# Performance work log

Hardware: AMD Instinct MI355X
Metric: run time of the kernel (lower is better)

The kernel has to match this reference:

```python
import jax, jax.numpy as jnp
import numpy as np

EPS = 1e-8

def _masked_mean_summary(h, m):
    # h: [B,D,Nx,T], m: [B,1,Nx,T] -> s: [B,Nx,D]
    msum = jnp.clip(jnp.sum(m, axis=-1), 1.0, None)          # [B,1,Nx]
    s = jnp.sum(h * m, axis=-1) / msum                       # [B,D,Nx]
    return jnp.transpose(s, (0, 2, 1))                       # [B,Nx,D]

def _cosine_alpha(s, prototypes):
    # s: [B,Nx,D], prototypes: [K,D] -> softmax cosine sims [B,Nx,K]
    s_n = s / jnp.clip(jnp.linalg.norm(s, axis=-1, keepdims=True), 1e-12, None)
    p_n = prototypes / jnp.clip(jnp.linalg.norm(prototypes, axis=-1, keepdims=True), 1e-12, None)
    sim = jnp.einsum('bnd,kd->bnk', s_n, p_n)
    return jax.nn.softmax(sim, axis=-1)

def setup_inputs() -> dict:
    key = jax.random.key(0)
    k1, k2, k3 = jax.random.split(key, 3)
    B, D, N, T = 4, 64, 2048, 64
    N_obs, K = 1024, 32
    h_time = jax.random.normal(k1, (B, D, N, T), dtype=jnp.float32)
    mask = jax.random.uniform(k2, (B, 1, N, T), dtype=jnp.float32)
    idx_obs = jnp.arange(N_obs, dtype=jnp.int64)
    prototypes = jax.random.normal(k3, (K, D), dtype=jnp.float32)
    return {"h_time": h_time, "mask": mask, "idx_obs": idx_obs, "prototypes": prototypes}

def reference(h_time, mask, idx_obs, prototypes):
    B, D, N, T = h_time.shape
    # --- observed-node routing ---
    h_obs = h_time[:, :, idx_obs, :]                          # [B,D,No,T]
    mask_obs = mask[:, :, idx_obs, :]                         # [B,1,No,T]
    s_obs = _masked_mean_summary(h_obs, mask_obs)             # [B,No,D]
    alpha_obs = _cosine_alpha(s_obs, prototypes)              # [B,No,K]
    # --- prototype timeseries aggregation (fused broadcast-reduce) ---
    # torch materializes [B,K,D,No,T]; equivalent contraction over No:
    H_num = jnp.einsum('bnk,bdnt->bkdt', alpha_obs, h_obs)    # [B,K,D,T]
    # weights_sum over No is sum_n alpha (independent of t), clamp 1e-8
    denom = jnp.clip(jnp.sum(alpha_obs, axis=1), EPS, None)   # [B,K]
    H_prototypes = H_num / denom[:, :, None, None]            # [B,K,D,T]
    # --- impute unobserved nodes ---
    # compute summaries/routing for ALL nodes, then select unobserved slots
    s_all = _masked_mean_summary(h_time, mask)                # [B,N,D]
    alpha_all = _cosine_alpha(s_all, prototypes)              # [B,N,K]
    imputed = jnp.einsum('bnk,bkdt->bdnt', alpha_all, H_prototypes)  # [B,D,N,T]
    obs_node = jnp.zeros((N,), dtype=bool).at[idx_obs].set(True)
    h_spatial = jnp.where(obs_node[None, None, :, None], h_time, imputed)
    return h_spatial
```

## Files before the change

kernel.cpp:

```cpp
#include <hip/hip_runtime.h>

#define BB   4
#define DD   64
#define NN   2048
#define TT   64
#define NOBS 1024
#define KK   32
#define EPSF 1e-8f

#define S_OFF     0
#define ALPHA_OFF (BB*NN*DD)
#define HNUM_OFF  (ALPHA_OFF + BB*NN*KK)
#define FLAGS_OFF (HNUM_OFF + BB*KK*DD*TT)
#define DINV_OFF  (FLAGS_OFF + NN)

__device__ __forceinline__ int idx_stride(const int* idx) {
  return (idx[1] == 0 && idx[2] == 1) ? 2 : 1;
}

__global__ void k0_mark(const int* __restrict__ idx, int* __restrict__ flags) {
  int i = blockIdx.x * 256 + threadIdx.x;
  int st = idx_stride(idx);
  if (i < NOBS) flags[idx[i * st]] = 1;
}

__global__ __launch_bounds__(256) void k1_summary(
    const float* __restrict__ h, const float* __restrict__ mask,
    const int* __restrict__ flags, float* __restrict__ s,
    float* __restrict__ out) {
  int blk = blockIdx.x;
  int b = blk >> 11;
  int n = blk & (NN - 1);
  int tid = threadIdx.x;
  int lane = tid & 63;
  int w = tid >> 6;
  int tq = lane & 15;
  int dd = lane >> 4;

  const float4* m4 = reinterpret_cast<const float4*>(mask) + ((size_t)b * NN + n) * (TT / 4);
  float4 mv = m4[tq];
  float msum = mv.x + mv.y + mv.z + mv.w;
  #pragma unroll
  for (int off = 8; off; off >>= 1) msum += __shfl_xor(msum, off);
  msum = fmaxf(msum, 1.0f);
  const bool obs = flags[n] != 0;

  #pragma unroll
  for (int i = 0; i < 4; ++i) {
    int d = (w << 4) + (i << 2) + dd;
    size_t rowf4 = ((((size_t)b * DD + d) * NN + n) * TT) >> 2;
    float4 hv = reinterpret_cast<const float4*>(h)[rowf4 + tq];
    float dot = hv.x * mv.x + hv.y * mv.y + hv.z * mv.z + hv.w * mv.w;
    #pragma unroll
    for (int off = 8; off; off >>= 1) dot += __shfl_xor(dot, off);
    if (tq == 0) s[((size_t)b * NN + n) * DD + d] = dot / msum;
    if (obs) reinterpret_cast<float4*>(out)[rowf4 + tq] = hv;
  }
}

__global__ __launch_bounds__(256) void k2_alpha(
    const float* __restrict__ s, const float* __restrict__ proto,
    float* __restrict__ alpha) {
  __shared__ float pT[DD * 33];
  __shared__ float pn[KK];
  __shared__ float snL[4][DD];
  int tid = threadIdx.x;
  {
    int k0 = tid >> 6;
    int d = tid & 63;
    #pragma unroll
    for (int i = 0; i < 8; ++i) {
      int k = k0 + (i << 2);
      pT[d * 33 + k] = proto[k * DD + d];
    }
  }
  __syncthreads();
  if (tid < 32) {
    float nsq = 0.f;
    #pragma unroll 8
    for (int d = 0; d < DD; ++d) { float v = pT[d * 33 + tid]; nsq = fmaf(v, v, nsq); }
    pn[tid] = fmaxf(sqrtf(nsq), 1e-12f);
  }
  __syncthreads();
  for (int r = tid; r < DD * KK; r += 256) {
    int d = r >> 5, k = r & 31;
    pT[d * 33 + k] /= pn[k];
  }
  __syncthreads();

  int w = tid >> 6, lane = tid & 63;
  int blk = blockIdx.x;
  int b = blk >> 9;
  int n = ((blk & 511) << 2) + w;

  float sd = s[((size_t)b * NN + n) * DD + lane];
  float nsq = sd * sd;
  #pragma unroll
  for (int off = 32; off; off >>= 1) nsq += __shfl_xor(nsq, off);
  float sn = sd / fmaxf(sqrtf(nsq), 1e-12f);
  snL[w][lane] = sn;
  __syncthreads();

  if (lane < 32) {
    float sim = 0.f;
    #pragma unroll 8
    for (int d = 0; d < DD; ++d) sim = fmaf(snL[w][d], pT[d * 33 + lane], sim);
    float m = sim;
    #pragma unroll
    for (int off = 16; off; off >>= 1) m = fmaxf(m, __shfl_xor(m, off));
    float e = expf(sim - m);
    float sum = e;
    #pragma unroll
    for (int off = 16; off; off >>= 1) sum += __shfl_xor(sum, off);
    alpha[((size_t)b * NN + n) * KK + lane] = e / sum;
  }
}

__global__ __launch_bounds__(256) void k2b_dinv(
    const float* __restrict__ alpha, const int* __restrict__ idx,
    float* __restrict__ dinv) {
  __shared__ float red[4];
  int blk = blockIdx.x;
  int b = blk >> 5, k = blk & 31;
  int tid = threadIdx.x;
  int st = idx_stride(idx);
  float sum = 0.f;
  for (int i = tid; i < NOBS; i += 256) {
    int n = idx[i * st];
    sum += alpha[((size_t)b * NN + n) * KK + k];
  }
  #pragma unroll
  for (int off = 32; off; off >>= 1) sum += __shfl_xor(sum, off);
  if ((tid & 63) == 0) red[tid >> 6] = sum;
  __syncthreads();
  if (tid == 0) {
    float tot = red[0] + red[1] + red[2] + red[3];
    dinv[blk] = 1.0f / fmaxf(tot, EPSF);
  }
}

__global__ __launch_bounds__(256) void k3_hnum(
    const float* __restrict__ h, const float* __restrict__ alpha,
    const int* __restrict__ idx, float* __restrict__ hnum) {
  __shared__ float aL[256 * 33];
  __shared__ int nL[256];
  int blk = blockIdx.x;
  int sp = blk & 3;
  int d = (blk >> 2) & (DD - 1);
  int b = blk >> 8;
  int tid = threadIdx.x;
  int i0 = sp * 256;
  int st = idx_stride(idx);

  for (int r = tid; r < 256 * 32; r += 256) {
    int i = r >> 5, k = r & 31;
    int n = idx[(i0 + i) * st];
    if (k == 0) nL[i] = n;
    aL[i * 33 + k] = alpha[((size_t)b * NN + n) * KK + k];
  }
  __syncthreads();

  int lane = tid & 63, w = tid >> 6;
  int tq = lane & 15, iq = lane >> 4;
  float4 acc[8];
  #pragma unroll
  for (int j = 0; j < 8; ++j) acc[j] = make_float4(0.f, 0.f, 0.f, 0.f);

  const size_t hbase4 = (((size_t)b * DD + d) * NN * TT) >> 2;
  for (int i = 0; i < 256; i += 4) {
    int n = nL[i + iq];
    float4 hv = reinterpret_cast<const float4*>(h)[hbase4 + (size_t)n * (TT / 4) + tq];
    const float* ar = &aL[(i + iq) * 33 + w * 8];
    #pragma unroll
    for (int j = 0; j < 8; ++j) {
      float a = ar[j];
      acc[j].x = fmaf(a, hv.x, acc[j].x);
      acc[j].y = fmaf(a, hv.y, acc[j].y);
      acc[j].z = fmaf(a, hv.z, acc[j].z);
      acc[j].w = fmaf(a, hv.w, acc[j].w);
    }
  }
  #pragma unroll
  for (int j = 0; j < 8; ++j) {
    acc[j].x += __shfl_xor(acc[j].x, 16); acc[j].x += __shfl_xor(acc[j].x, 32);
    acc[j].y += __shfl_xor(acc[j].y, 16); acc[j].y += __shfl_xor(acc[j].y, 32);
    acc[j].z += __shfl_xor(acc[j].z, 16); acc[j].z += __shfl_xor(acc[j].z, 32);
    acc[j].w += __shfl_xor(acc[j].w, 16); acc[j].w += __shfl_xor(acc[j].w, 32);
  }
  if (iq == 0) {
    #pragma unroll
    for (int j = 0; j < 8; ++j) {
      int k = w * 8 + j;
      size_t o = (((size_t)b * KK + k) * DD + d) * TT + tq * 4;
      atomicAdd(&hnum[o + 0], acc[j].x);
      atomicAdd(&hnum[o + 1], acc[j].y);
      atomicAdd(&hnum[o + 2], acc[j].z);
      atomicAdd(&hnum[o + 3], acc[j].w);
    }
  }
}

__global__ __launch_bounds__(256) void k4_impute(
    const float* __restrict__ hnum, const float* __restrict__ alpha,
    const float* __restrict__ dinv, const int* __restrict__ flags,
    float* __restrict__ out) {
  __shared__ float aL[8][KK];
  __shared__ int fL[8];
  int blk = blockIdx.x;
  int b = blk >> 8;
  int n0 = (blk & 255) << 3;
  int tid = threadIdx.x;
  {
    int j = tid >> 5, k = tid & 31;
    aL[j][k] = alpha[((size_t)b * NN + n0 + j) * KK + k] * dinv[b * KK + k];
  }
  if (tid < 8) fL[tid] = flags[n0 + tid];
  __syncthreads();
  if (fL[0] & fL[1] & fL[2] & fL[3] & fL[4] & fL[5] & fL[6] & fL[7]) return;

  int tl = tid & 15;
  int dslot = tid >> 4;
  const float4* hb = reinterpret_cast<const float4*>(hnum);
  #pragma unroll
  for (int it = 0; it < 4; ++it) {
    int d = dslot + (it << 4);
    float4 acc[8];
    #pragma unroll
    for (int j = 0; j < 8; ++j) acc[j] = make_float4(0.f, 0.f, 0.f, 0.f);
    #pragma unroll
    for (int k = 0; k < KK; k += 4) {
      float4 h0 = hb[(((size_t)b * KK + k    ) * DD + d) * (TT / 4) + tl];
      float4 h1 = hb[(((size_t)b * KK + k + 1) * DD + d) * (TT / 4) + tl];
      float4 h2 = hb[(((size_t)b * KK + k + 2) * DD + d) * (TT / 4) + tl];
      float4 h3 = hb[(((size_t)b * KK + k + 3) * DD + d) * (TT / 4) + tl];
      #pragma unroll
      for (int j = 0; j < 8; ++j) {
        float4 av = *reinterpret_cast<const float4*>(&aL[j][k]);
        acc[j].x = fmaf(av.x, h0.x, fmaf(av.y, h1.x, fmaf(av.z, h2.x, fmaf(av.w, h3.x, acc[j].x))));
        acc[j].y = fmaf(av.x, h0.y, fmaf(av.y, h1.y, fmaf(av.z, h2.y, fmaf(av.w, h3.y, acc[j].y))));
        acc[j].z = fmaf(av.x, h0.z, fmaf(av.y, h1.z, fmaf(av.z, h2.z, fmaf(av.w, h3.z, acc[j].z))));
        acc[j].w = fmaf(av.x, h0.w, fmaf(av.y, h1.w, fmaf(av.z, h2.w, fmaf(av.w, h3.w, acc[j].w))));
      }
    }
    #pragma unroll
    for (int j = 0; j < 8; ++j) {
      if (!fL[j]) {
        size_t o4 = ((((size_t)b * DD + d) * NN + (n0 + j)) * TT) >> 2;
        reinterpret_cast<float4*>(out)[o4 + tl] = acc[j];
      }
    }
  }
}

extern "C" void kernel_launch(void* const* d_in, const int* in_sizes, int n_in,
                              void* d_out, int out_size, void* d_ws, size_t ws_size,
                              hipStream_t stream) {
  const float* h     = (const float*)d_in[0];
  const float* mask  = (const float*)d_in[1];
  const int*   idx   = (const int*)d_in[2];
  const float* proto = (const float*)d_in[3];
  float* out = (float*)d_out;
  float* ws  = (float*)d_ws;

  float* s     = ws + S_OFF;
  float* alpha = ws + ALPHA_OFF;
  float* hnum  = ws + HNUM_OFF;
  int*   flags = (int*)(ws + FLAGS_OFF);
  float* dinv  = ws + DINV_OFF;

  hipMemsetAsync(hnum, 0, (size_t)(BB * KK * DD * TT + NN) * sizeof(float), stream);
  k0_mark<<<(NOBS + 255) / 256, 256, 0, stream>>>(idx, flags);
  k1_summary<<<BB * NN, 256, 0, stream>>>(h, mask, flags, s, out);
  k2_alpha<<<BB * (NN / 4), 256, 0, stream>>>(s, proto, alpha);
  k2b_dinv<<<BB * KK, 256, 0, stream>>>(alpha, idx, dinv);
  k3_hnum<<<BB * DD * 4, 256, 0, stream>>>(h, alpha, idx, hnum);
  k4_impute<<<BB * (NN / 8), 256, 0, stream>>>(hnum, alpha, dinv, flags, out);
}
```

Measured before the change: 324.8 us.

## Compact unobserved nodes and keep prototype rows in registers during imputation

```diff
diff --git a/kernel.cpp b/kernel.cpp
--- a/kernel.cpp
+++ b/kernel.cpp
@@ -7,12 +7,15 @@
 #define NOBS 1024
 #define KK   32
 #define EPSF 1e-8f
+#define CHUNK 64
 
 #define S_OFF     0
 #define ALPHA_OFF (BB*NN*DD)
 #define HNUM_OFF  (ALPHA_OFF + BB*NN*KK)
 #define FLAGS_OFF (HNUM_OFF + BB*KK*DD*TT)
 #define DINV_OFF  (FLAGS_OFF + NN)
+#define LIST_OFF  (DINV_OFF + BB*KK)
+#define NUN_OFF   (LIST_OFF + NN)
 
 __device__ __forceinline__ int idx_stride(const int* idx) {
   return (idx[1] == 0 && idx[2] == 1) ? 2 : 1;
@@ -22,6 +25,34 @@
   int i = blockIdx.x * 256 + threadIdx.x;
   int st = idx_stride(idx);
   if (i < NOBS) flags[idx[i * st]] = 1;
+}
+
+__global__ __launch_bounds__(256) void k0b_compact(
+    const int* __restrict__ flags, int* __restrict__ list, int* __restrict__ nunp) {
+  __shared__ int wsum[4];
+  int tid = threadIdx.x;
+  int base = tid * 8;
+  int cnt = 0;
+  int loc[8];
+  #pragma unroll
+  for (int i = 0; i < 8; ++i) {
+    int n = base + i;
+    if (!flags[n]) loc[cnt++] = n;
+  }
+  int lane = tid & 63, w = tid >> 6;
+  int scan = cnt;
+  #pragma unroll
+  for (int off = 1; off < 64; off <<= 1) {
+    int v = __shfl_up(scan, off);
+    if (lane >= off) scan += v;
+  }
+  if (lane == 63) wsum[w] = scan;
+  __syncthreads();
+  int wbase = 0;
+  for (int i = 0; i < w; ++i) wbase += wsum[i];
+  int excl = wbase + scan - cnt;
+  for (int i = 0; i < cnt; ++i) list[excl + i] = loc[i];
+  if (tid == 255) nunp[0] = wbase + scan;
 }
 
 __global__ __launch_bounds__(256) void k1_summary(
@@ -202,53 +233,52 @@
 
 __global__ __launch_bounds__(256) void k4_impute(
     const float* __restrict__ hnum, const float* __restrict__ alpha,
-    const float* __restrict__ dinv, const int* __restrict__ flags,
-    float* __restrict__ out) {
-  __shared__ float aL[8][KK];
-  __shared__ int fL[8];
-  int blk = blockIdx.x;
-  int b = blk >> 8;
-  int n0 = (blk & 255) << 3;
-  int tid = threadIdx.x;
-  {
-    int j = tid >> 5, k = tid & 31;
-    aL[j][k] = alpha[((size_t)b * NN + n0 + j) * KK + k] * dinv[b * KK + k];
-  }
-  if (tid < 8) fL[tid] = flags[n0 + tid];
-  __syncthreads();
-  if (fL[0] & fL[1] & fL[2] & fL[3] & fL[4] & fL[5] & fL[6] & fL[7]) return;
-
+    const float* __restrict__ dinv, const int* __restrict__ list,
+    const int* __restrict__ nunp, float* __restrict__ out) {
+  __shared__ float wL[CHUNK][KK];
+  __shared__ int ndL[CHUNK];
+  int blk = blockIdx.x;
+  int c  = blk & 31;
+  int dg = (blk >> 5) & 3;
+  int b  = blk >> 7;
+  int nun = nunp[0];
+  int n0 = c * CHUNK;
+  if (n0 >= nun) return;
+  int cnt = min(CHUNK, nun - n0);
+
+  int tid = threadIdx.x;
   int tl = tid & 15;
   int dslot = tid >> 4;
-  const float4* hb = reinterpret_cast<const float4*>(hnum);
-  #pragma unroll
-  for (int it = 0; it < 4; ++it) {
-    int d = dslot + (it << 4);
-    float4 acc[8];
-    #pragma unroll
-    for (int j = 0; j < 8; ++j) acc[j] = make_float4(0.f, 0.f, 0.f, 0.f);
-    #pragma unroll
-    for (int k = 0; k < KK; k += 4) {
-      float4 h0 = hb[(((size_t)b * KK + k    ) * DD + d) * (TT / 4) + tl];
-      float4 h1 = hb[(((size_t)b * KK + k + 1) * DD + d) * (TT / 4) + tl];
-      float4 h2 = hb[(((size_t)b * KK + k + 2) * DD + d) * (TT / 4) + tl];
-      float4 h3 = hb[(((size_t)b * KK + k + 3) * DD + d) * (TT / 4) + tl];
-      #pragma unroll
-      for (int j = 0; j < 8; ++j) {
-        float4 av = *reinterpret_cast<const float4*>(&aL[j][k]);
-        acc[j].x = fmaf(av.x, h0.x, fmaf(av.y, h1.x, fmaf(av.z, h2.x, fmaf(av.w, h3.x, acc[j].x))));
-        acc[j].y = fmaf(av.x, h0.y, fmaf(av.y, h1.y, fmaf(av.z, h2.y, fmaf(av.w, h3.y, acc[j].y))));
-        acc[j].z = fmaf(av.x, h0.z, fmaf(av.y, h1.z, fmaf(av.z, h2.z, fmaf(av.w, h3.z, acc[j].z))));
-        acc[j].w = fmaf(av.x, h0.w, fmaf(av.y, h1.w, fmaf(av.z, h2.w, fmaf(av.w, h3.w, acc[j].w))));
-      }
+  int d = dg * 16 + dslot;
+
+  for (int r = tid; r < cnt * KK; r += 256) {
+    int j = r >> 5, k = r & 31;
+    int node = list[n0 + j];
+    if (k == 0) ndL[j] = node;
+    wL[j][k] = alpha[((size_t)b * NN + node) * KK + k] * dinv[b * KK + k];
+  }
+
+  float4 hreg[KK];
+  const float4* hb = reinterpret_cast<const float4*>(hnum) + (size_t)b * KK * DD * (TT / 4);
+  #pragma unroll
+  for (int k = 0; k < KK; ++k) hreg[k] = hb[((size_t)k * DD + d) * (TT / 4) + tl];
+
+  __syncthreads();
+
+  float4* out4 = reinterpret_cast<float4*>(out);
+  for (int j = 0; j < cnt; ++j) {
+    float4 acc = make_float4(0.f, 0.f, 0.f, 0.f);
+    #pragma unroll
+    for (int kq = 0; kq < KK / 4; ++kq) {
+      float4 wv = *reinterpret_cast<const float4*>(&wL[j][kq * 4]);
+      float4 h0 = hreg[kq * 4 + 0], h1 = hreg[kq * 4 + 1];
+      float4 h2 = hreg[kq * 4 + 2], h3 = hreg[kq * 4 + 3];
+      acc.x = fmaf(wv.x, h0.x, fmaf(wv.y, h1.x, fmaf(wv.z, h2.x, fmaf(wv.w, h3.x, acc.x))));
+      acc.y = fmaf(wv.x, h0.y, fmaf(wv.y, h1.y, fmaf(wv.z, h2.y, fmaf(wv.w, h3.y, acc.y))));
+      acc.z = fmaf(wv.x, h0.z, fmaf(wv.y, h1.z, fmaf(wv.z, h2.z, fmaf(wv.w, h3.z, acc.z))));
+      acc.w = fmaf(wv.x, h0.w, fmaf(wv.y, h1.w, fmaf(wv.z, h2.w, fmaf(wv.w, h3.w, acc.w))));
     }
-    #pragma unroll
-    for (int j = 0; j < 8; ++j) {
-      if (!fL[j]) {
-        size_t o4 = ((((size_t)b * DD + d) * NN + (n0 + j)) * TT) >> 2;
-        reinterpret_cast<float4*>(out)[o4 + tl] = acc[j];
-      }
-    }
+    out4[(((size_t)b * DD + d) * NN + ndL[j]) * (TT / 4) + tl] = acc;
   }
 }
 
@@ -267,12 +297,15 @@
   float* hnum  = ws + HNUM_OFF;
   int*   flags = (int*)(ws + FLAGS_OFF);
   float* dinv  = ws + DINV_OFF;
+  int*   list  = (int*)(ws + LIST_OFF);
+  int*   nunp  = (int*)(ws + NUN_OFF);
 
   hipMemsetAsync(hnum, 0, (size_t)(BB * KK * DD * TT + NN) * sizeof(float), stream);
   k0_mark<<<(NOBS + 255) / 256, 256, 0, stream>>>(idx, flags);
+  k0b_compact<<<1, 256, 0, stream>>>(flags, list, nunp);
   k1_summary<<<BB * NN, 256, 0, stream>>>(h, mask, flags, s, out);
   k2_alpha<<<BB * (NN / 4), 256, 0, stream>>>(s, proto, alpha);
   k2b_dinv<<<BB * KK, 256, 0, stream>>>(alpha, idx, dinv);
   k3_hnum<<<BB * DD * 4, 256, 0, stream>>>(h, alpha, idx, hnum);
-  k4_impute<<<BB * (NN / 8), 256, 0, stream>>>(hnum, alpha, dinv, flags, out);
-}
+  k4_impute<<<BB * 4 * (NN / CHUNK), 256, 0, stream>>>(hnum, alpha, dinv, list, nunp, out);
+}
```

Result: no change. 328.2 us (+1.0%).

## Fuse summary with alpha and move observed-row copy into impute kernel

Applied to the files above, without the earlier changes.

```diff
diff --git a/kernel.cpp b/kernel.cpp
--- a/kernel.cpp
+++ b/kernel.cpp
@@ -8,9 +8,8 @@
 #define KK   32
 #define EPSF 1e-8f
 
-#define S_OFF     0
-#define ALPHA_OFF (BB*NN*DD)
-#define HNUM_OFF  (ALPHA_OFF + BB*NN*KK)
+#define ALPHA_OFF 0
+#define HNUM_OFF  (BB*NN*KK)
 #define FLAGS_OFF (HNUM_OFF + BB*KK*DD*TT)
 #define DINV_OFF  (FLAGS_OFF + NN)
 
@@ -18,102 +17,93 @@
   return (idx[1] == 0 && idx[2] == 1) ? 2 : 1;
 }
 
-__global__ void k0_mark(const int* __restrict__ idx, int* __restrict__ flags) {
-  int i = blockIdx.x * 256 + threadIdx.x;
+__global__ __launch_bounds__(256) void k0_flags(const int* __restrict__ idx,
+                                                int* __restrict__ flags) {
+  int tid = threadIdx.x;
   int st = idx_stride(idx);
-  if (i < NOBS) flags[idx[i * st]] = 1;
-}
-
-__global__ __launch_bounds__(256) void k1_summary(
+  #pragma unroll
+  for (int i = 0; i < 8; ++i) flags[tid * 8 + i] = 0;
+  __threadfence();
+  __syncthreads();
+  #pragma unroll
+  for (int i = 0; i < 4; ++i) flags[idx[(tid + i * 256) * st]] = 1;
+}
+
+__global__ __launch_bounds__(256) void k1_alpha(
     const float* __restrict__ h, const float* __restrict__ mask,
-    const int* __restrict__ flags, float* __restrict__ s,
-    float* __restrict__ out) {
-  int blk = blockIdx.x;
-  int b = blk >> 11;
-  int n = blk & (NN - 1);
-  int tid = threadIdx.x;
-  int lane = tid & 63;
-  int w = tid >> 6;
-  int tq = lane & 15;
-  int dd = lane >> 4;
-
-  const float4* m4 = reinterpret_cast<const float4*>(mask) + ((size_t)b * NN + n) * (TT / 4);
-  float4 mv = m4[tq];
-  float msum = mv.x + mv.y + mv.z + mv.w;
-  #pragma unroll
-  for (int off = 8; off; off >>= 1) msum += __shfl_xor(msum, off);
-  msum = fmaxf(msum, 1.0f);
-  const bool obs = flags[n] != 0;
-
-  #pragma unroll
-  for (int i = 0; i < 4; ++i) {
-    int d = (w << 4) + (i << 2) + dd;
-    size_t rowf4 = ((((size_t)b * DD + d) * NN + n) * TT) >> 2;
-    float4 hv = reinterpret_cast<const float4*>(h)[rowf4 + tq];
-    float dot = hv.x * mv.x + hv.y * mv.y + hv.z * mv.z + hv.w * mv.w;
-    #pragma unroll
-    for (int off = 8; off; off >>= 1) dot += __shfl_xor(dot, off);
-    if (tq == 0) s[((size_t)b * NN + n) * DD + d] = dot / msum;
-    if (obs) reinterpret_cast<float4*>(out)[rowf4 + tq] = hv;
-  }
-}
-
-__global__ __launch_bounds__(256) void k2_alpha(
-    const float* __restrict__ s, const float* __restrict__ proto,
-    float* __restrict__ alpha) {
+    const float* __restrict__ proto, float* __restrict__ alpha) {
+  __shared__ float sL[16][65];
   __shared__ float pT[DD * 33];
   __shared__ float pn[KK];
-  __shared__ float snL[4][DD];
-  int tid = threadIdx.x;
-  {
-    int k0 = tid >> 6;
-    int d = tid & 63;
-    #pragma unroll
-    for (int i = 0; i < 8; ++i) {
-      int k = k0 + (i << 2);
-      pT[d * 33 + k] = proto[k * DD + d];
-    }
-  }
-  __syncthreads();
+  int blk = blockIdx.x;
+  int b = blk >> 7;
+  int n0 = (blk & 127) << 4;
+  int tid = threadIdx.x;
+  int ns = tid >> 4;
+  int tq = tid & 15;
+
+  float4 mv = reinterpret_cast<const float4*>(mask)[((size_t)b * NN + n0 + ns) * (TT / 4) + tq];
+  float msum = mv.x + mv.y + mv.z + mv.w;
+  #pragma unroll
+  for (int off = 8; off; off >>= 1) msum += __shfl_xor(msum, off);
+  float minv = 1.0f / fmaxf(msum, 1.0f);
+
+  for (int r = tid; r < KK * 16; r += 256) {
+    int k = r >> 4, dq = r & 15;
+    float4 pv = reinterpret_cast<const float4*>(proto)[k * 16 + dq];
+    pT[(dq * 4 + 0) * 33 + k] = pv.x;
+    pT[(dq * 4 + 1) * 33 + k] = pv.y;
+    pT[(dq * 4 + 2) * 33 + k] = pv.z;
+    pT[(dq * 4 + 3) * 33 + k] = pv.w;
+  }
+
+  for (int d = 0; d < DD; ++d) {
+    float4 hv = reinterpret_cast<const float4*>(h)[(((size_t)b * DD + d) * NN + n0 + ns) * (TT / 4) + tq];
+    float dot = hv.x * mv.x + hv.y * mv.y + hv.z * mv.z + hv.w * mv.w;
+    #pragma unroll
+    for (int off = 8; off; off >>= 1) dot += __shfl_xor(dot, off);
+    if (tq == 0) sL[ns][d] = dot * minv;
+  }
+  __syncthreads();
+
   if (tid < 32) {
-    float nsq = 0.f;
+    float q = 0.f;
     #pragma unroll 8
-    for (int d = 0; d < DD; ++d) { float v = pT[d * 33 + tid]; nsq = fmaf(v, v, nsq); }
-    pn[tid] = fmaxf(sqrtf(nsq), 1e-12f);
+    for (int d = 0; d < DD; ++d) { float v = pT[d * 33 + tid]; q = fmaf(v, v, q); }
+    pn[tid] = fmaxf(sqrtf(q), 1e-12f);
   }
   __syncthreads();
   for (int r = tid; r < DD * KK; r += 256) {
     int d = r >> 5, k = r & 31;
     pT[d * 33 + k] /= pn[k];
   }
-  __syncthreads();
-
-  int w = tid >> 6, lane = tid & 63;
-  int blk = blockIdx.x;
-  int b = blk >> 9;
-  int n = ((blk & 511) << 2) + w;
-
-  float sd = s[((size_t)b * NN + n) * DD + lane];
-  float nsq = sd * sd;
-  #pragma unroll
-  for (int off = 32; off; off >>= 1) nsq += __shfl_xor(nsq, off);
-  float sn = sd / fmaxf(sqrtf(nsq), 1e-12f);
-  snL[w][lane] = sn;
-  __syncthreads();
-
-  if (lane < 32) {
-    float sim = 0.f;
-    #pragma unroll 8
-    for (int d = 0; d < DD; ++d) sim = fmaf(snL[w][d], pT[d * 33 + lane], sim);
-    float m = sim;
-    #pragma unroll
-    for (int off = 16; off; off >>= 1) m = fmaxf(m, __shfl_xor(m, off));
-    float e = expf(sim - m);
-    float sum = e;
-    #pragma unroll
-    for (int off = 16; off; off >>= 1) sum += __shfl_xor(sum, off);
-    alpha[((size_t)b * NN + n) * KK + lane] = e / sum;
-  }
+  float q = 0.f;
+  #pragma unroll
+  for (int i = 0; i < 4; ++i) { float v = sL[ns][tq + 16 * i]; q = fmaf(v, v, q); }
+  #pragma unroll
+  for (int off = 8; off; off >>= 1) q += __shfl_xor(q, off);
+  float sinv = 1.0f / fmaxf(sqrtf(q), 1e-12f);
+  __syncthreads();
+
+  int klo = tq, khi = tq + 16;
+  float s0 = 0.f, s1 = 0.f;
+  #pragma unroll 8
+  for (int d = 0; d < DD; ++d) {
+    float sv = sL[ns][d] * sinv;
+    s0 = fmaf(sv, pT[d * 33 + klo], s0);
+    s1 = fmaf(sv, pT[d * 33 + khi], s1);
+  }
+  float m = fmaxf(s0, s1);
+  #pragma unroll
+  for (int off = 8; off; off >>= 1) m = fmaxf(m, __shfl_xor(m, off));
+  float e0 = expf(s0 - m), e1 = expf(s1 - m);
+  float sum = e0 + e1;
+  #pragma unroll
+  for (int off = 8; off; off >>= 1) sum += __shfl_xor(sum, off);
+  float rinv = 1.0f / sum;
+  size_t ao = ((size_t)b * NN + n0 + ns) * KK;
+  alpha[ao + klo] = e0 * rinv;
+  alpha[ao + khi] = e1 * rinv;
 }
 
 __global__ __launch_bounds__(256) void k2b_dinv(
@@ -200,54 +190,61 @@
   }
 }
 
-__global__ __launch_bounds__(256) void k4_impute(
-    const float* __restrict__ hnum, const float* __restrict__ alpha,
-    const float* __restrict__ dinv, const int* __restrict__ flags,
-    float* __restrict__ out) {
-  __shared__ float aL[8][KK];
-  __shared__ int fL[8];
-  int blk = blockIdx.x;
-  int b = blk >> 8;
-  int n0 = (blk & 255) << 3;
-  int tid = threadIdx.x;
-  {
-    int j = tid >> 5, k = tid & 31;
-    aL[j][k] = alpha[((size_t)b * NN + n0 + j) * KK + k] * dinv[b * KK + k];
-  }
-  if (tid < 8) fL[tid] = flags[n0 + tid];
-  __syncthreads();
-  if (fL[0] & fL[1] & fL[2] & fL[3] & fL[4] & fL[5] & fL[6] & fL[7]) return;
-
-  int tl = tid & 15;
-  int dslot = tid >> 4;
+__global__ __launch_bounds__(256) void k4_final(
+    const float* __restrict__ h, const float* __restrict__ hnum,
+    const float* __restrict__ alpha, const float* __restrict__ dinv,
+    const int* __restrict__ flags, float* __restrict__ out) {
+  __shared__ float wL[64][36];
+  __shared__ int fL[512];
+  int blk = blockIdx.x;
+  int qn = blk & 3;
+  int d  = (blk >> 2) & (DD - 1);
+  int b  = blk >> 8;
+  int tid = threadIdx.x;
+  int ns = tid >> 4;
+  int tq = tid & 15;
+  int nstart = qn * 512;
+
+  for (int i = tid; i < 512; i += 256) fL[i] = flags[nstart + i];
+
+  float4 hn[KK];
   const float4* hb = reinterpret_cast<const float4*>(hnum);
   #pragma unroll
-  for (int it = 0; it < 4; ++it) {
-    int d = dslot + (it << 4);
-    float4 acc[8];
-    #pragma unroll
-    for (int j = 0; j < 8; ++j) acc[j] = make_float4(0.f, 0.f, 0.f, 0.f);
-    #pragma unroll
-    for (int k = 0; k < KK; k += 4) {
-      float4 h0 = hb[(((size_t)b * KK + k    ) * DD + d) * (TT / 4) + tl];
-      float4 h1 = hb[(((size_t)b * KK + k + 1) * DD + d) * (TT / 4) + tl];
-      float4 h2 = hb[(((size_t)b * KK + k + 2) * DD + d) * (TT / 4) + tl];
-      float4 h3 = hb[(((size_t)b * KK + k + 3) * DD + d) * (TT / 4) + tl];
+  for (int k = 0; k < KK; ++k) {
+    float4 v = hb[(((size_t)b * KK + k) * DD + d) * (TT / 4) + tq];
+    float dv = dinv[b * KK + k];
+    hn[k] = make_float4(v.x * dv, v.y * dv, v.z * dv, v.w * dv);
+  }
+
+  const float4* h4 = reinterpret_cast<const float4*>(h);
+  float4* o4 = reinterpret_cast<float4*>(out);
+  const float4* a4 = reinterpret_cast<const float4*>(alpha);
+  size_t rowbase = (((size_t)b * DD + d) * NN + nstart) * (TT / 4);
+
+  for (int tile = 0; tile < 8; ++tile) {
+    __syncthreads();
+    for (int r = tid; r < 512; r += 256) {
+      int j = r >> 3, kq = r & 7;
+      float4 av = a4[((size_t)b * NN + nstart + tile * 64 + j) * 8 + kq];
+      *reinterpret_cast<float4*>(&wL[j][kq * 4]) = av;
+    }
+    __syncthreads();
+    #pragma unroll
+    for (int sub = 0; sub < 4; ++sub) {
+      int nl = tile * 64 + sub * 16 + ns;
+      float4 hv = h4[rowbase + (size_t)nl * (TT / 4) + tq];
+      float4 acc = make_float4(0.f, 0.f, 0.f, 0.f);
+      const float* wr = &wL[sub * 16 + ns][0];
       #pragma unroll
-      for (int j = 0; j < 8; ++j) {
-        float4 av = *reinterpret_cast<const float4*>(&aL[j][k]);
-        acc[j].x = fmaf(av.x, h0.x, fmaf(av.y, h1.x, fmaf(av.z, h2.x, fmaf(av.w, h3.x, acc[j].x))));
-        acc[j].y = fmaf(av.x, h0.y, fmaf(av.y, h1.y, fmaf(av.z, h2.y, fmaf(av.w, h3.y, acc[j].y))));
-        acc[j].z = fmaf(av.x, h0.z, fmaf(av.y, h1.z, fmaf(av.z, h2.z, fmaf(av.w, h3.z, acc[j].z))));
-        acc[j].w = fmaf(av.x, h0.w, fmaf(av.y, h1.w, fmaf(av.z, h2.w, fmaf(av.w, h3.w, acc[j].w))));
+      for (int kq = 0; kq < 8; ++kq) {
+        float4 wv = *reinterpret_cast<const float4*>(wr + kq * 4);
+        acc.x = fmaf(wv.x, hn[4*kq].x, fmaf(wv.y, hn[4*kq+1].x, fmaf(wv.z, hn[4*kq+2].x, fmaf(wv.w, hn[4*kq+3].x, acc.x))));
+        acc.y = fmaf(wv.x, hn[4*kq].y, fmaf(wv.y, hn[4*kq+1].y, fmaf(wv.z, hn[4*kq+2].y, fmaf(wv.w, hn[4*kq+3].y, acc.y))));
+        acc.z = fmaf(wv.x, hn[4*kq].z, fmaf(wv.y, hn[4*kq+1].z, fmaf(wv.z, hn[4*kq+2].z, fmaf(wv.w, hn[4*kq+3].z, acc.z))));
+        acc.w = fmaf(wv.x, hn[4*kq].w, fmaf(wv.y, hn[4*kq+1].w, fmaf(wv.z, hn[4*kq+2].w, fmaf(wv.w, hn[4*kq+3].w, acc.w))));
       }
-    }
-    #pragma unroll
-    for (int j = 0; j < 8; ++j) {
-      if (!fL[j]) {
-        size_t o4 = ((((size_t)b * DD + d) * NN + (n0 + j)) * TT) >> 2;
-        reinterpret_cast<float4*>(out)[o4 + tl] = acc[j];
-      }
+      float4 res = fL[nl] ? hv : acc;
+      o4[rowbase + (size_t)nl * (TT / 4) + tq] = res;
     }
   }
 }
@@ -262,17 +259,15 @@
   float* out = (float*)d_out;
   float* ws  = (float*)d_ws;
 
-  float* s     = ws + S_OFF;
   float* alpha = ws + ALPHA_OFF;
   float* hnum  = ws + HNUM_OFF;
   int*   flags = (int*)(ws + FLAGS_OFF);
   float* dinv  = ws + DINV_OFF;
 
-  hipMemsetAsync(hnum, 0, (size_t)(BB * KK * DD * TT + NN) * sizeof(float), stream);
-  k0_mark<<<(NOBS + 255) / 256, 256, 0, stream>>>(idx, flags);
-  k1_summary<<<BB * NN, 256, 0, stream>>>(h, mask, flags, s, out);
-  k2_alpha<<<BB * (NN / 4), 256, 0, stream>>>(s, proto, alpha);
+  hipMemsetAsync(hnum, 0, (size_t)(BB * KK * DD * TT) * sizeof(float), stream);
+  k0_flags<<<1, 256, 0, stream>>>(idx, flags);
+  k1_alpha<<<BB * (NN / 16), 256, 0, stream>>>(h, mask, proto, alpha);
   k2b_dinv<<<BB * KK, 256, 0, stream>>>(alpha, idx, dinv);
   k3_hnum<<<BB * DD * 4, 256, 0, stream>>>(h, alpha, idx, hnum);
-  k4_impute<<<BB * (NN / 8), 256, 0, stream>>>(hnum, alpha, dinv, flags, out);
-}
+  k4_final<<<BB * DD * 4, 256, 0, stream>>>(h, hnum, alpha, dinv, flags, out);
+}
```

After: 330.4 us. Within noise of the previous version (+1.7%).
